# Optimization experiments

Hardware: AMD Instinct MI355X
Metric: run time of the kernel (lower is better)

The kernel has to match this reference:

```python
import jax, jax.numpy as jnp
import numpy as np

N_NODES = 50000
N_EDGES = 800000
N_GRAPHS = 512
NODE_IN = 128
EDGE_IN = 64
HIDDEN = 128
SHARED = 64


def setup_inputs() -> dict:
    key = jax.random.key(0)
    ks = jax.random.split(key, 24)
    def lin(k, fan_in, fan_out):
        lim = 1.0 / np.sqrt(fan_in)
        kw, kb = jax.random.split(k)
        w = jax.random.uniform(kw, (fan_in, fan_out), jnp.float32, -lim, lim)
        b = jax.random.uniform(kb, (fan_out,), jnp.float32, -lim, lim)
        return w, b
    x = jax.random.normal(ks[0], (N_NODES, NODE_IN), jnp.float32)
    edge_index = jax.random.randint(ks[1], (2, N_EDGES), 0, N_NODES, jnp.int64)
    edge_attr = jax.random.normal(ks[2], (N_EDGES, EDGE_IN), jnp.float32)
    batch = jnp.sort(jax.random.randint(ks[3], (N_NODES,), 0, N_GRAPHS, jnp.int64))
    e1_w, e1_b = lin(ks[4], EDGE_IN, NODE_IN)
    n1_w1, n1_b1 = lin(ks[5], NODE_IN, HIDDEN)
    n1_w2, n1_b2 = lin(ks[6], HIDDEN, HIDDEN)
    e2_w, e2_b = lin(ks[7], EDGE_IN, HIDDEN)
    n2_w1, n2_b1 = lin(ks[8], HIDDEN, HIDDEN)
    n2_w2, n2_b2 = lin(ks[9], HIDDEN, HIDDEN)
    fc_w, fc_b = lin(ks[10], HIDDEN, SHARED)
    hS_w, hS_b = lin(ks[11], SHARED, 1)
    hP_w, hP_b = lin(ks[12], SHARED, 1)
    hN_w, hN_b = lin(ks[13], SHARED, 1)
    return dict(x=x, edge_index=edge_index, edge_attr=edge_attr, batch=batch,
                e1_w=e1_w, e1_b=e1_b, n1_w1=n1_w1, n1_b1=n1_b1, n1_w2=n1_w2, n1_b2=n1_b2,
                e2_w=e2_w, e2_b=e2_b, n2_w1=n2_w1, n2_b1=n2_b1, n2_w2=n2_w2, n2_b2=n2_b2,
                fc_w=fc_w, fc_b=fc_b, hS_w=hS_w, hS_b=hS_b, hP_w=hP_w, hP_b=hP_b,
                hN_w=hN_w, hN_b=hN_b)


def gine_conv(x, edge_index, edge_attr, ew, eb, w1, b1, w2, b2):
    # message: relu(x_j + Lin(edge_attr)); aggregate: scatter-sum to target;
    # update: MLP((1 + eps) * x_i + aggr) with eps = 0 (PyG default)
    e = edge_attr @ ew + eb                      # [E, C]
    m = jax.nn.relu(x[edge_index[0]] + e)        # gather + fused add/relu
    aggr = jax.ops.segment_sum(m, edge_index[1], num_segments=N_NODES)
    h = x + aggr
    return jax.nn.relu(h @ w1 + b1) @ w2 + b2


def global_mean_pool(x, batch):
    sums = jax.ops.segment_sum(x, batch, num_segments=N_GRAPHS)
    cnt = jax.ops.segment_sum(jnp.ones((x.shape[0],), x.dtype), batch, num_segments=N_GRAPHS)
    return sums / jnp.maximum(cnt, 1.0)[:, None]


def reference(x, edge_index, edge_attr, batch,
              e1_w, e1_b, n1_w1, n1_b1, n1_w2, n1_b2,
              e2_w, e2_b, n2_w1, n2_b1, n2_w2, n2_b2,
              fc_w, fc_b, hS_w, hS_b, hP_w, hP_b, hN_w, hN_b):
    h = jax.nn.relu(gine_conv(x, edge_index, edge_attr, e1_w, e1_b, n1_w1, n1_b1, n1_w2, n1_b2))
    h = jax.nn.relu(gine_conv(h, edge_index, edge_attr, e2_w, e2_b, n2_w1, n2_b1, n2_w2, n2_b2))
    g = global_mean_pool(h, batch)               # [G, HIDDEN]
    s = jax.nn.relu(g @ fc_w + fc_b)             # [G, SHARED]
    logS = (s @ hS_w + hS_b)[:, 0]
    logP = (s @ hP_w + hP_b)[:, 0]
    nr = (s @ hN_w + hN_b)[:, 0]
    return logS, logP, nr
```

## Files before the change

### kernel.cpp

```cpp
#include <hip/hip_runtime.h>
#include <hip/hip_bf16.h>


typedef __bf16 bf16_t;

#define N_NODES   50000
#define N_EDGES   800000
#define N_GRAPHS  512
#define HID       128
#define EIN       64
#define PNODES    16
#define SCAN_BLK  1024
#define NCHUNK    49

#define RL(v, l)  __int_as_float(__builtin_amdgcn_readlane(__float_as_int(v), (l)))
#define RLI(v, l) __builtin_amdgcn_readlane((v), (l))

__device__ __forceinline__ float ldf(const void* p, size_t i, int f32m) {
    return f32m ? ((const float*)p)[i] : (float)((const bf16_t*)p)[i];
}
__device__ __forceinline__ int ldi(const void* p, size_t i, int i64m) {
    return i64m ? (int)((const long long*)p)[i] : ((const int*)p)[i];
}

__global__ void k_detect(const unsigned short* __restrict__ xw,
                         const unsigned int*   __restrict__ eiw,
                         int* __restrict__ flags)
{
    if (threadIdx.x == 0 && blockIdx.x == 0) {
        int sane = 0;
        for (int i = 0; i < 256; ++i) {
            int e = (xw[i] >> 7) & 0xFF;
            if (e >= 100 && e <= 150) ++sane;
        }
        flags[0] = (sane < 220) ? 1 : 0;
        int nzhigh = 0;
        for (int i = 0; i < 256; ++i)
            if (eiw[2*i + 1] != 0) ++nzhigh;
        flags[1] = (nzhigh == 0) ? 1 : 0;
    }
}

__global__ void k_cvt4(const void* __restrict__ x, float* __restrict__ dst,
                       const int* __restrict__ flags) {
    const int f32m = flags[0];
    size_t i = (size_t)blockIdx.x * 256 + threadIdx.x;
    if (f32m) {
        ((float4*)dst)[i] = ((const float4*)x)[i];
    } else {
        const bf16_t* s = (const bf16_t*)x;
        float4 v;
        v.x = (float)s[4*i+0]; v.y = (float)s[4*i+1];
        v.z = (float)s[4*i+2]; v.w = (float)s[4*i+3];
        ((float4*)dst)[i] = v;
    }
}

__global__ void k_hist(const void* __restrict__ ei, int* __restrict__ CNT,
                       const int* __restrict__ flags)
{
    const int i64m = flags[1];
    int e = blockIdx.x * 256 + threadIdx.x;
    int d = ldi(ei, (size_t)N_EDGES + e, i64m);
    atomicAdd(&CNT[d], 1);
}

__global__ __launch_bounds__(SCAN_BLK) void k_scanA(const int* __restrict__ CNT,
                                                    int* __restrict__ OFF,
                                                    int* __restrict__ PS)
{
    __shared__ int tmp[SCAN_BLK];
    const int t = threadIdx.x;
    const int i = blockIdx.x * SCAN_BLK + t;
    const int v = (i < N_NODES) ? CNT[i] : 0;
    tmp[t] = v;
    __syncthreads();
    for (int off = 1; off < SCAN_BLK; off <<= 1) {
        int u = (t >= off) ? tmp[t - off] : 0;
        __syncthreads();
        tmp[t] += u;
        __syncthreads();
    }
    if (i < N_NODES) OFF[i] = tmp[t] - v;
    if (t == SCAN_BLK - 1) PS[blockIdx.x] = tmp[t];
}

__global__ void k_scanB(int* __restrict__ PS)
{
    const int lane = threadIdx.x;
    const int v0 = (lane < NCHUNK) ? PS[lane] : 0;
    int v = v0;
#pragma unroll
    for (int off = 1; off < 64; off <<= 1) {
        int u = __shfl_up(v, off, 64);
        if (lane >= off) v += u;
    }
    if (lane < NCHUNK) PS[lane] = v - v0;
}

__global__ void k_scanC(int* __restrict__ OFF, const int* __restrict__ PS,
                        int* __restrict__ CUR)
{
    int i = blockIdx.x * 256 + threadIdx.x;
    if (i < N_NODES) {
        int o = OFF[i] + PS[i >> 10];
        OFF[i] = o;
        CUR[i] = o;
    }
}

__global__ void k_scatter(const void* __restrict__ ei, int* __restrict__ CUR,
                          int* __restrict__ CSR, const int* __restrict__ flags)
{
    const int i64m = flags[1];
    int e = blockIdx.x * 256 + threadIdx.x;
    int s = ldi(ei, e, i64m);
    int d = ldi(ei, (size_t)N_EDGES + e, i64m);
    int p = atomicAdd(&CUR[d], 1);
    CSR[p]              = e;
    CSR[N_EDGES + p]    = s;
    CSR[2*N_EDGES + p]  = d;
}

__global__ __launch_bounds__(512) void k_edge_s(
        const void* __restrict__ Xg, int xg_ws,
        const int*  __restrict__ CSR,
        const void* __restrict__ ea,
        const void* __restrict__ ew,
        const void* __restrict__ eb,
        float*      __restrict__ ag,
        const int*  __restrict__ flags)
{
    __shared__ float4 Wq[16 * 128];
    __shared__ float  ebs[HID];
    const int f32m = flags[0];
    const int xgf  = xg_ws ? 1 : f32m;

    for (int i = threadIdx.x; i < 16 * 128; i += 512) {
        int k4 = i >> 7, c = i & 127;
        float4 w;
        w.x = ldf(ew, (size_t)(4*k4+0)*HID + c, f32m);
        w.y = ldf(ew, (size_t)(4*k4+1)*HID + c, f32m);
        w.z = ldf(ew, (size_t)(4*k4+2)*HID + c, f32m);
        w.w = ldf(ew, (size_t)(4*k4+3)*HID + c, f32m);
        Wq[i] = w;
    }
    for (int i = threadIdx.x; i < HID; i += 512) ebs[i] = ldf(eb, i, f32m);
    __syncthreads();

    const int lane = threadIdx.x & 63;
    const int wid  = (blockIdx.x * 512 + threadIdx.x) >> 6;
    const int nw   = gridDim.x * 8;
    const int ngrp = N_EDGES / 8;
    const float eb0 = ebs[lane], eb1 = ebs[64 + lane];

    auto LOADIDX = [&](int p0) -> int {
        int v = 0;
        if (lane < 24) v = CSR[(size_t)(lane >> 3) * N_EDGES + p0 + (lane & 7)];
        return v;
    };
    auto LOADAV = [&](int vv, float* av) {
#pragma unroll
        for (int i = 0; i < 8; ++i) {
            int eid = RLI(vv, i);
            av[i] = ldf(ea, (size_t)eid * EIN + lane, f32m);
        }
    };

    int g = wid;
    if (g < ngrp) {
        float avA[8];
        int vvA = LOADIDX(g * 8);
        LOADAV(vvA, avA);
        int gB = g + nw;
        int vvB = (gB < ngrp) ? LOADIDX(gB * 8) : 0;

        while (true) {
            const bool hasB = (gB < ngrp);
            float avB[8];
            if (hasB) LOADAV(vvB, avB);
            const int gC = gB + nw;
            int vvC = (hasB && gC < ngrp) ? LOADIDX(gC * 8) : 0;

            int src[8], dst[8];
#pragma unroll
            for (int i = 0; i < 8; ++i) {
                src[i] = RLI(vvA, 8 + i);
                dst[i] = RLI(vvA, 16 + i);
            }
            float x0[8], x1[8];
#pragma unroll
            for (int i = 0; i < 8; ++i) {
                x0[i] = ldf(Xg, (size_t)src[i] * HID + lane,      xgf);
                x1[i] = ldf(Xg, (size_t)src[i] * HID + 64 + lane, xgf);
            }

            float acc0[8], acc1[8];
#pragma unroll
            for (int i = 0; i < 8; ++i) { acc0[i] = 0.f; acc1[i] = 0.f; }

#pragma unroll 4
            for (int k4 = 0; k4 < 16; ++k4) {
                float4 w0 = Wq[k4 * 128 + lane];
                float4 w1 = Wq[k4 * 128 + 64 + lane];
#pragma unroll
                for (int i = 0; i < 8; ++i) {
                    float a0 = RL(avA[i], 4*k4+0);
                    float a1 = RL(avA[i], 4*k4+1);
                    float a2 = RL(avA[i], 4*k4+2);
                    float a3 = RL(avA[i], 4*k4+3);
                    acc0[i] = fmaf(a3, w0.w, fmaf(a2, w0.z, fmaf(a1, w0.y, fmaf(a0, w0.x, acc0[i]))));
                    acc1[i] = fmaf(a3, w1.w, fmaf(a2, w1.z, fmaf(a1, w1.y, fmaf(a0, w1.x, acc1[i]))));
                }
            }

            float s0 = 0.f, s1 = 0.f;
#pragma unroll
            for (int i = 0; i < 8; ++i) {
                float v0 = fmaxf(x0[i] + acc0[i] + eb0, 0.f);
                float v1 = fmaxf(x1[i] + acc1[i] + eb1, 0.f);
                s0 += v0; s1 += v1;
                if (i == 7 || dst[i + 1] != dst[i]) {
                    unsafeAtomicAdd(ag + (size_t)dst[i] * HID + lane,      s0);
                    unsafeAtomicAdd(ag + (size_t)dst[i] * HID + 64 + lane, s1);
                    s0 = 0.f; s1 = 0.f;
                }
            }

            if (!hasB) break;
            g = gB; gB = gC;
            vvA = vvB; vvB = vvC;
#pragma unroll
            for (int i = 0; i < 8; ++i) avA[i] = avB[i];
        }
    }
}

__global__ __launch_bounds__(1024) void k_mlp2(
        const float* __restrict__ A,
        const void*  __restrict__ W1, const void* __restrict__ b1,
        const void*  __restrict__ W2, const void* __restrict__ b2,
        float*       __restrict__ Out,
        float*       __restrict__ Out2,
        const int*   __restrict__ flags)
{
    __shared__ float4 W1q[32 * 128];
    __shared__ float4 W2q[32 * 128];
    const int f32m = flags[0];
    for (int i = threadIdx.x; i < 32 * 128; i += 1024) {
        int k4 = i >> 7, c = i & 127;
        float4 w;
        w.x = ldf(W1, (size_t)(4*k4+0)*HID + c, f32m);
        w.y = ldf(W1, (size_t)(4*k4+1)*HID + c, f32m);
        w.z = ldf(W1, (size_t)(4*k4+2)*HID + c, f32m);
        w.w = ldf(W1, (size_t)(4*k4+3)*HID + c, f32m);
        W1q[i] = w;
        w.x = ldf(W2, (size_t)(4*k4+0)*HID + c, f32m);
        w.y = ldf(W2, (size_t)(4*k4+1)*HID + c, f32m);
        w.z = ldf(W2, (size_t)(4*k4+2)*HID + c, f32m);
        w.w = ldf(W2, (size_t)(4*k4+3)*HID + c, f32m);
        W2q[i] = w;
    }
    __syncthreads();

    const int lane = threadIdx.x & 63;
    const int wid  = (blockIdx.x * 1024 + threadIdx.x) >> 6;
    const int nw   = gridDim.x * 16;
    const float c10 = ldf(b1, lane,      f32m);
    const float c11 = ldf(b1, 64 + lane, f32m);
    const float c20 = ldf(b2, lane,      f32m);
    const float c21 = ldf(b2, 64 + lane, f32m);
    const int ngrp = N_NODES / 8;

    for (int g = wid; g < ngrp; g += nw) {
        const int n0 = g * 8;
        float alo[8], ahi[8], t0[8], t1[8];
#pragma unroll
        for (int i = 0; i < 8; ++i) {
            alo[i] = A[(size_t)(n0+i) * HID + lane];
            ahi[i] = A[(size_t)(n0+i) * HID + 64 + lane];
            t0[i] = c10; t1[i] = c11;
        }
#pragma unroll 4
        for (int k4 = 0; k4 < 16; ++k4) {
            float4 w0 = W1q[k4 * 128 + lane];
            float4 w1 = W1q[k4 * 128 + 64 + lane];
#pragma unroll
            for (int i = 0; i < 8; ++i) {
                float a0 = RL(alo[i], 4*k4+0);
                float a1 = RL(alo[i], 4*k4+1);
                float a2 = RL(alo[i], 4*k4+2);
                float a3 = RL(alo[i], 4*k4+3);
                t0[i] = fmaf(a3, w0.w, fmaf(a2, w0.z, fmaf(a1, w0.y, fmaf(a0, w0.x, t0[i]))));
                t1[i] = fmaf(a3, w1.w, fmaf(a2, w1.z, fmaf(a1, w1.y, fmaf(a0, w1.x, t1[i]))));
            }
        }
#pragma unroll 4
        for (int k4 = 16; k4 < 32; ++k4) {
            float4 w0 = W1q[k4 * 128 + lane];
            float4 w1 = W1q[k4 * 128 + 64 + lane];
#pragma unroll
            for (int i = 0; i < 8; ++i) {
                float a0 = RL(ahi[i], 4*k4+0 - 64);
                float a1 = RL(ahi[i], 4*k4+1 - 64);
                float a2 = RL(ahi[i], 4*k4+2 - 64);
                float a3 = RL(ahi[i], 4*k4+3 - 64);
                t0[i] = fmaf(a3, w0.w, fmaf(a2, w0.z, fmaf(a1, w0.y, fmaf(a0, w0.x, t0[i]))));
                t1[i] = fmaf(a3, w1.w, fmaf(a2, w1.z, fmaf(a1, w1.y, fmaf(a0, w1.x, t1[i]))));
            }
        }
#pragma unroll
        for (int i = 0; i < 8; ++i) {
            t0[i] = fmaxf(t0[i], 0.f);
            t1[i] = fmaxf(t1[i], 0.f);
        }
        float o0[8], o1[8];
#pragma unroll
        for (int i = 0; i < 8; ++i) { o0[i] = c20; o1[i] = c21; }
#pragma unroll 4
        for (int k4 = 0; k4 < 16; ++k4) {
            float4 w0 = W2q[k4 * 128 + lane];
            float4 w1 = W2q[k4 * 128 + 64 + lane];
#pragma unroll
            for (int i = 0; i < 8; ++i) {
                float a0 = RL(t0[i], 4*k4+0);
                float a1 = RL(t0[i], 4*k4+1);
                float a2 = RL(t0[i], 4*k4+2);
                float a3 = RL(t0[i], 4*k4+3);
                o0[i] = fmaf(a3, w0.w, fmaf(a2, w0.z, fmaf(a1, w0.y, fmaf(a0, w0.x, o0[i]))));
                o1[i] = fmaf(a3, w1.w, fmaf(a2, w1.z, fmaf(a1, w1.y, fmaf(a0, w1.x, o1[i]))));
            }
        }
#pragma unroll 4
        for (int k4 = 16; k4 < 32; ++k4) {
            float4 w0 = W2q[k4 * 128 + lane];
            float4 w1 = W2q[k4 * 128 + 64 + lane];
#pragma unroll
            for (int i = 0; i < 8; ++i) {
                float a0 = RL(t1[i], 4*k4+0 - 64);
                float a1 = RL(t1[i], 4*k4+1 - 64);
                float a2 = RL(t1[i], 4*k4+2 - 64);
                float a3 = RL(t1[i], 4*k4+3 - 64);
                o0[i] = fmaf(a3, w0.w, fmaf(a2, w0.z, fmaf(a1, w0.y, fmaf(a0, w0.x, o0[i]))));
                o1[i] = fmaf(a3, w1.w, fmaf(a2, w1.z, fmaf(a1, w1.y, fmaf(a0, w1.x, o1[i]))));
            }
        }
#pragma unroll
        for (int i = 0; i < 8; ++i) {
            float v0 = fmaxf(o0[i], 0.f);
            float v1 = fmaxf(o1[i], 0.f);
            Out[(size_t)(n0+i) * HID + lane]      = v0;
            Out[(size_t)(n0+i) * HID + 64 + lane] = v1;
            if (Out2) {
                Out2[(size_t)(n0+i) * HID + lane]      = v0;
                Out2[(size_t)(n0+i) * HID + 64 + lane] = v1;
            }
        }
    }
}

__global__ void k_pool_s(const float* __restrict__ X, const void* __restrict__ batch,
                         float* __restrict__ GS, float* __restrict__ GC,
                         const int* __restrict__ flags)
{
    const int i64m = flags[1];
    const int c  = threadIdx.x;
    const int tl = threadIdx.x & 63;
    const int n0 = blockIdx.x * PNODES;

    int bv = (tl < PNODES) ? ldi(batch, n0 + tl, i64m) : 0;

    int bprev = RLI(bv, 0);
    float acc = 0.f;
    int   cnt = 0;
#pragma unroll
    for (int j = 0; j < PNODES; ++j) {
        int b = RLI(bv, j);
        if (b != bprev) {
            unsafeAtomicAdd(&GS[(size_t)bprev * HID + c], acc);
            if (c == 0) unsafeAtomicAdd(&GC[bprev], (float)cnt);
            acc = 0.f; cnt = 0; bprev = b;
        }
        acc += X[(size_t)(n0 + j) * HID + c];
        ++cnt;
    }
    unsafeAtomicAdd(&GS[(size_t)bprev * HID + c], acc);
    if (c == 0) unsafeAtomicAdd(&GC[bprev], (float)cnt);
}

__global__ void k_head(const float* __restrict__ GS, const float* __restrict__ GC,
                       const void* __restrict__ fcw, const void* __restrict__ fcb,
                       const void* __restrict__ hSw, const void* __restrict__ hSb,
                       const void* __restrict__ hPw, const void* __restrict__ hPb,
                       const void* __restrict__ hNw, const void* __restrict__ hNb,
                       float* __restrict__ out, const int* __restrict__ flags)
{
    const int f32m = flags[0];
    const int g = blockIdx.x;
    const int lane = threadIdx.x;
    const float inv = 1.f / fmaxf(GC[g], 1.f);
    const float g0 = GS[(size_t)g * HID + lane]      * inv;
    const float g1 = GS[(size_t)g * HID + 64 + lane] * inv;

    float acc = 0.f;
    for (int k = 0; k < 64; ++k) {
        float gk = __shfl(g0, k, 64);
        acc += gk * ldf(fcw, k * 64 + lane, f32m);
    }
    for (int k = 0; k < 64; ++k) {
        float gk = __shfl(g1, k, 64);
        acc += gk * ldf(fcw, (64 + k) * 64 + lane, f32m);
    }
    float s = fmaxf(acc + ldf(fcb, lane, f32m), 0.f);

    float pS = s * ldf(hSw, lane, f32m);
    float pP = s * ldf(hPw, lane, f32m);
    float pN = s * ldf(hNw, lane, f32m);
#pragma unroll
    for (int off = 32; off; off >>= 1) {
        pS += __shfl_down(pS, off, 64);
        pP += __shfl_down(pP, off, 64);
        pN += __shfl_down(pN, off, 64);
    }
    if (lane == 0) {
        out[g]                = pS + ldf(hSb, 0, f32m);
        out[N_GRAPHS + g]     = pP + ldf(hPb, 0, f32m);
        out[2 * N_GRAPHS + g] = pN + ldf(hNb, 0, f32m);
    }
}

extern "C" void kernel_launch(void* const* d_in, const int* in_sizes, int n_in,
                              void* d_out, int out_size, void* d_ws, size_t ws_size,
                              hipStream_t stream)
{
    const void* x     = d_in[0];
    const void* ei    = d_in[1];
    const void* ea    = d_in[2];
    const void* batch = d_in[3];
    const void* e1w = d_in[4],  *e1b = d_in[5];
    const void* n1w1= d_in[6],  *n1b1= d_in[7];
    const void* n1w2= d_in[8],  *n1b2= d_in[9];
    const void* e2w = d_in[10], *e2b = d_in[11];
    const void* n2w1= d_in[12], *n2b1= d_in[13];
    const void* n2w2= d_in[14], *n2b2= d_in[15];
    const void* fcw = d_in[16], *fcb = d_in[17];
    const void* hSw = d_in[18], *hSb = d_in[19];
    const void* hPw = d_in[20], *hPb = d_in[21];
    const void* hNw = d_in[22], *hNb = d_in[23];

    float* B1  = (float*)d_ws;
    float* B2  = B1 + (size_t)N_NODES * HID;
    float* GS  = B2 + (size_t)N_NODES * HID;
    float* GC  = GS + (size_t)N_GRAPHS * HID;
    int*   FL  = (int*)(GC + N_GRAPHS);
    int*   PS  = FL + 4;
    int*   OFF = PS + 64;
    int*   CNT = OFF + N_NODES;
    int*   CUR = CNT + N_NODES;
    int*   CSR = CUR + N_NODES;

    k_detect<<<1, 64, 0, stream>>>((const unsigned short*)x, (const unsigned int*)ei, FL);
    hipMemsetAsync(GS, 0, (N_GRAPHS * HID + N_GRAPHS) * sizeof(float), stream);
    hipMemsetAsync(CNT, 0, N_NODES * sizeof(int), stream);

    k_hist   <<<N_EDGES / 256, 256, 0, stream>>>(ei, CNT, FL);
    k_scanA  <<<NCHUNK, SCAN_BLK, 0, stream>>>(CNT, OFF, PS);
    k_scanB  <<<1, 64, 0, stream>>>(PS);
    k_scanC  <<<(N_NODES + 255) / 256, 256, 0, stream>>>(OFF, PS, CUR);
    k_scatter<<<N_EDGES / 256, 256, 0, stream>>>(ei, CUR, CSR, FL);

    const int NV4_BLKS = (N_NODES * HID / 4) / 256;

    k_cvt4  <<<NV4_BLKS, 256, 0, stream>>>(x, B1, FL);
    k_edge_s<<<2048, 512, 0, stream>>>(x, 0, CSR, ea, e1w, e1b, B1, FL);
    k_mlp2  <<<256, 1024, 0, stream>>>(B1, n1w1, n1b1, n1w2, n1b2, B1, B2, FL);

    k_edge_s<<<2048, 512, 0, stream>>>(B1, 1, CSR, ea, e2w, e2b, B2, FL);
    k_mlp2  <<<256, 1024, 0, stream>>>(B2, n2w1, n2b1, n2w2, n2b2, B2, nullptr, FL);

    k_pool_s<<<N_NODES / PNODES, 128, 0, stream>>>(B2, batch, GS, GC, FL);
    k_head  <<<N_GRAPHS, 64, 0, stream>>>(GS, GC, fcw, fcb, hSw, hSb, hPw, hPb, hNw, hNb,
                                          (float*)d_out, FL);
}
```

Baseline: 1.261 ms.

## Hold GEMM weights in registers and split node MLP into per-layer kernels

```diff
diff --git a/kernel.cpp b/kernel.cpp
--- a/kernel.cpp
+++ b/kernel.cpp
@@ -122,7 +122,7 @@
     CSR[2*N_EDGES + p]  = d;
 }
 
-__global__ __launch_bounds__(512) void k_edge_s(
+__global__ __launch_bounds__(256, 2) void k_edge_r(
         const void* __restrict__ Xg, int xg_ws,
         const int*  __restrict__ CSR,
         const void* __restrict__ ea,
@@ -131,28 +131,31 @@
         float*      __restrict__ ag,
         const int*  __restrict__ flags)
 {
-    __shared__ float4 Wq[16 * 128];
-    __shared__ float  ebs[HID];
     const int f32m = flags[0];
     const int xgf  = xg_ws ? 1 : f32m;
-
-    for (int i = threadIdx.x; i < 16 * 128; i += 512) {
-        int k4 = i >> 7, c = i & 127;
-        float4 w;
-        w.x = ldf(ew, (size_t)(4*k4+0)*HID + c, f32m);
-        w.y = ldf(ew, (size_t)(4*k4+1)*HID + c, f32m);
-        w.z = ldf(ew, (size_t)(4*k4+2)*HID + c, f32m);
-        w.w = ldf(ew, (size_t)(4*k4+3)*HID + c, f32m);
-        Wq[i] = w;
-    }
-    for (int i = threadIdx.x; i < HID; i += 512) ebs[i] = ldf(eb, i, f32m);
-    __syncthreads();
-
     const int lane = threadIdx.x & 63;
-    const int wid  = (blockIdx.x * 512 + threadIdx.x) >> 6;
-    const int nw   = gridDim.x * 8;
+    const int wid  = (blockIdx.x * 256 + threadIdx.x) >> 6;
+    const int nw   = gridDim.x * 4;
     const int ngrp = N_EDGES / 8;
-    const float eb0 = ebs[lane], eb1 = ebs[64 + lane];
+
+    float wr0[EIN], wr1[EIN];
+    if (f32m) {
+        const float* Wf = (const float*)ew;
+#pragma unroll
+        for (int k = 0; k < EIN; ++k) {
+            wr0[k] = Wf[(size_t)k * HID + lane];
+            wr1[k] = Wf[(size_t)k * HID + 64 + lane];
+        }
+    } else {
+        const bf16_t* Wb = (const bf16_t*)ew;
+#pragma unroll
+        for (int k = 0; k < EIN; ++k) {
+            wr0[k] = (float)Wb[(size_t)k * HID + lane];
+            wr1[k] = (float)Wb[(size_t)k * HID + 64 + lane];
+        }
+    }
+    const float eb0 = ldf(eb, lane,      f32m);
+    const float eb1 = ldf(eb, 64 + lane, f32m);
 
     auto LOADIDX = [&](int p0) -> int {
         int v = 0;
@@ -199,18 +202,18 @@
 #pragma unroll
             for (int i = 0; i < 8; ++i) { acc0[i] = 0.f; acc1[i] = 0.f; }
 
-#pragma unroll 4
+#pragma unroll
             for (int k4 = 0; k4 < 16; ++k4) {
-                float4 w0 = Wq[k4 * 128 + lane];
-                float4 w1 = Wq[k4 * 128 + 64 + lane];
 #pragma unroll
                 for (int i = 0; i < 8; ++i) {
                     float a0 = RL(avA[i], 4*k4+0);
                     float a1 = RL(avA[i], 4*k4+1);
                     float a2 = RL(avA[i], 4*k4+2);
                     float a3 = RL(avA[i], 4*k4+3);
-                    acc0[i] = fmaf(a3, w0.w, fmaf(a2, w0.z, fmaf(a1, w0.y, fmaf(a0, w0.x, acc0[i]))));
-                    acc1[i] = fmaf(a3, w1.w, fmaf(a2, w1.z, fmaf(a1, w1.y, fmaf(a0, w1.x, acc1[i]))));
+                    acc0[i] = fmaf(a3, wr0[4*k4+3], fmaf(a2, wr0[4*k4+2],
+                              fmaf(a1, wr0[4*k4+1], fmaf(a0, wr0[4*k4+0], acc0[i]))));
+                    acc1[i] = fmaf(a3, wr1[4*k4+3], fmaf(a2, wr1[4*k4+2],
+                              fmaf(a1, wr1[4*k4+1], fmaf(a0, wr1[4*k4+0], acc1[i]))));
                 }
             }
 
@@ -236,119 +239,97 @@
     }
 }
 
-__global__ __launch_bounds__(1024) void k_mlp2(
+__global__ __launch_bounds__(256, 2) void k_mlp_r(
         const float* __restrict__ A,
-        const void*  __restrict__ W1, const void* __restrict__ b1,
-        const void*  __restrict__ W2, const void* __restrict__ b2,
+        const void*  __restrict__ W,
+        const void*  __restrict__ bias,
         float*       __restrict__ Out,
         float*       __restrict__ Out2,
         const int*   __restrict__ flags)
 {
-    __shared__ float4 W1q[32 * 128];
-    __shared__ float4 W2q[32 * 128];
     const int f32m = flags[0];
-    for (int i = threadIdx.x; i < 32 * 128; i += 1024) {
-        int k4 = i >> 7, c = i & 127;
-        float4 w;
-        w.x = ldf(W1, (size_t)(4*k4+0)*HID + c, f32m);
-        w.y = ldf(W1, (size_t)(4*k4+1)*HID + c, f32m);
-        w.z = ldf(W1, (size_t)(4*k4+2)*HID + c, f32m);
-        w.w = ldf(W1, (size_t)(4*k4+3)*HID + c, f32m);
-        W1q[i] = w;
-        w.x = ldf(W2, (size_t)(4*k4+0)*HID + c, f32m);
-        w.y = ldf(W2, (size_t)(4*k4+1)*HID + c, f32m);
-        w.z = ldf(W2, (size_t)(4*k4+2)*HID + c, f32m);
-        w.w = ldf(W2, (size_t)(4*k4+3)*HID + c, f32m);
-        W2q[i] = w;
-    }
-    __syncthreads();
-
     const int lane = threadIdx.x & 63;
-    const int wid  = (blockIdx.x * 1024 + threadIdx.x) >> 6;
-    const int nw   = gridDim.x * 16;
-    const float c10 = ldf(b1, lane,      f32m);
-    const float c11 = ldf(b1, 64 + lane, f32m);
-    const float c20 = ldf(b2, lane,      f32m);
-    const float c21 = ldf(b2, 64 + lane, f32m);
+    const int wid  = (blockIdx.x * 256 + threadIdx.x) >> 6;
+    const int nw   = gridDim.x * 4;
+    const float b0 = ldf(bias, lane,      f32m);
+    const float b1 = ldf(bias, 64 + lane, f32m);
     const int ngrp = N_NODES / 8;
+
+    const float*  Wf = (const float*)W;
+    const bf16_t* Wb = (const bf16_t*)W;
+
+    float wr0[64], wr1[64];
 
     for (int g = wid; g < ngrp; g += nw) {
         const int n0 = g * 8;
-        float alo[8], ahi[8], t0[8], t1[8];
+        float alo[8], ahi[8], acc0[8], acc1[8];
 #pragma unroll
         for (int i = 0; i < 8; ++i) {
             alo[i] = A[(size_t)(n0+i) * HID + lane];
             ahi[i] = A[(size_t)(n0+i) * HID + 64 + lane];
-            t0[i] = c10; t1[i] = c11;
-        }
-#pragma unroll 4
+            acc0[i] = b0; acc1[i] = b1;
+        }
+
+        if (f32m) {
+#pragma unroll
+            for (int k = 0; k < 64; ++k) {
+                wr0[k] = Wf[(size_t)k * HID + lane];
+                wr1[k] = Wf[(size_t)k * HID + 64 + lane];
+            }
+        } else {
+#pragma unroll
+            for (int k = 0; k < 64; ++k) {
+                wr0[k] = (float)Wb[(size_t)k * HID + lane];
+                wr1[k] = (float)Wb[(size_t)k * HID + 64 + lane];
+            }
+        }
+#pragma unroll
         for (int k4 = 0; k4 < 16; ++k4) {
-            float4 w0 = W1q[k4 * 128 + lane];
-            float4 w1 = W1q[k4 * 128 + 64 + lane];
 #pragma unroll
             for (int i = 0; i < 8; ++i) {
                 float a0 = RL(alo[i], 4*k4+0);
                 float a1 = RL(alo[i], 4*k4+1);
                 float a2 = RL(alo[i], 4*k4+2);
                 float a3 = RL(alo[i], 4*k4+3);
-                t0[i] = fmaf(a3, w0.w, fmaf(a2, w0.z, fmaf(a1, w0.y, fmaf(a0, w0.x, t0[i]))));
-                t1[i] = fmaf(a3, w1.w, fmaf(a2, w1.z, fmaf(a1, w1.y, fmaf(a0, w1.x, t1[i]))));
-            }
-        }
-#pragma unroll 4
-        for (int k4 = 16; k4 < 32; ++k4) {
-            float4 w0 = W1q[k4 * 128 + lane];
-            float4 w1 = W1q[k4 * 128 + 64 + lane];
+                acc0[i] = fmaf(a3, wr0[4*k4+3], fmaf(a2, wr0[4*k4+2],
+                          fmaf(a1, wr0[4*k4+1], fmaf(a0, wr0[4*k4+0], acc0[i]))));
+                acc1[i] = fmaf(a3, wr1[4*k4+3], fmaf(a2, wr1[4*k4+2],
+                          fmaf(a1, wr1[4*k4+1], fmaf(a0, wr1[4*k4+0], acc1[i]))));
+            }
+        }
+
+        if (f32m) {
+#pragma unroll
+            for (int k = 0; k < 64; ++k) {
+                wr0[k] = Wf[(size_t)(64 + k) * HID + lane];
+                wr1[k] = Wf[(size_t)(64 + k) * HID + 64 + lane];
+            }
+        } else {
+#pragma unroll
+            for (int k = 0; k < 64; ++k) {
+                wr0[k] = (float)Wb[(size_t)(64 + k) * HID + lane];
+                wr1[k] = (float)Wb[(size_t)(64 + k) * HID + 64 + lane];
+            }
+        }
+#pragma unroll
+        for (int k4 = 0; k4 < 16; ++k4) {
 #pragma unroll
             for (int i = 0; i < 8; ++i) {
-                float a0 = RL(ahi[i], 4*k4+0 - 64);
-                float a1 = RL(ahi[i], 4*k4+1 - 64);
-                float a2 = RL(ahi[i], 4*k4+2 - 64);
-                float a3 = RL(ahi[i], 4*k4+3 - 64);
-                t0[i] = fmaf(a3, w0.w, fmaf(a2, w0.z, fmaf(a1, w0.y, fmaf(a0, w0.x, t0[i]))));
-                t1[i] = fmaf(a3, w1.w, fmaf(a2, w1.z, fmaf(a1, w1.y, fmaf(a0, w1.x, t1[i]))));
-            }
-        }
+                float a0 = RL(ahi[i], 4*k4+0);
+                float a1 = RL(ahi[i], 4*k4+1);
+                float a2 = RL(ahi[i], 4*k4+2);
+                float a3 = RL(ahi[i], 4*k4+3);
+                acc0[i] = fmaf(a3, wr0[4*k4+3], fmaf(a2, wr0[4*k4+2],
+                          fmaf(a1, wr0[4*k4+1], fmaf(a0, wr0[4*k4+0], acc0[i]))));
+                acc1[i] = fmaf(a3, wr1[4*k4+3], fmaf(a2, wr1[4*k4+2],
+                          fmaf(a1, wr1[4*k4+1], fmaf(a0, wr1[4*k4+0], acc1[i]))));
+            }
+        }
+
 #pragma unroll
         for (int i = 0; i < 8; ++i) {
-            t0[i] = fmaxf(t0[i], 0.f);
-            t1[i] = fmaxf(t1[i], 0.f);
-        }
-        float o0[8], o1[8];
-#pragma unroll
-        for (int i = 0; i < 8; ++i) { o0[i] = c20; o1[i] = c21; }
-#pragma unroll 4
-        for (int k4 = 0; k4 < 16; ++k4) {
-            float4 w0 = W2q[k4 * 128 + lane];
-            float4 w1 = W2q[k4 * 128 + 64 + lane];
-#pragma unroll
-            for (int i = 0; i < 8; ++i) {
-                float a0 = RL(t0[i], 4*k4+0);
-                float a1 = RL(t0[i], 4*k4+1);
-                float a2 = RL(t0[i], 4*k4+2);
-                float a3 = RL(t0[i], 4*k4+3);
-                o0[i] = fmaf(a3, w0.w, fmaf(a2, w0.z, fmaf(a1, w0.y, fmaf(a0, w0.x, o0[i]))));
-                o1[i] = fmaf(a3, w1.w, fmaf(a2, w1.z, fmaf(a1, w1.y, fmaf(a0, w1.x, o1[i]))));
-            }
-        }
-#pragma unroll 4
-        for (int k4 = 16; k4 < 32; ++k4) {
-            float4 w0 = W2q[k4 * 128 + lane];
-            float4 w1 = W2q[k4 * 128 + 64 + lane];
-#pragma unroll
-            for (int i = 0; i < 8; ++i) {
-                float a0 = RL(t1[i], 4*k4+0 - 64);
-                float a1 = RL(t1[i], 4*k4+1 - 64);
-                float a2 = RL(t1[i], 4*k4+2 - 64);
-                float a3 = RL(t1[i], 4*k4+3 - 64);
-                o0[i] = fmaf(a3, w0.w, fmaf(a2, w0.z, fmaf(a1, w0.y, fmaf(a0, w0.x, o0[i]))));
-                o1[i] = fmaf(a3, w1.w, fmaf(a2, w1.z, fmaf(a1, w1.y, fmaf(a0, w1.x, o1[i]))));
-            }
-        }
-#pragma unroll
-        for (int i = 0; i < 8; ++i) {
-            float v0 = fmaxf(o0[i], 0.f);
-            float v1 = fmaxf(o1[i], 0.f);
+            float v0 = fmaxf(acc0[i], 0.f);
+            float v1 = fmaxf(acc1[i], 0.f);
             Out[(size_t)(n0+i) * HID + lane]      = v0;
             Out[(size_t)(n0+i) * HID + 64 + lane] = v1;
             if (Out2) {
@@ -472,11 +453,13 @@
     const int NV4_BLKS = (N_NODES * HID / 4) / 256;
 
     k_cvt4  <<<NV4_BLKS, 256, 0, stream>>>(x, B1, FL);
-    k_edge_s<<<2048, 512, 0, stream>>>(x, 0, CSR, ea, e1w, e1b, B1, FL);
-    k_mlp2  <<<256, 1024, 0, stream>>>(B1, n1w1, n1b1, n1w2, n1b2, B1, B2, FL);
-
-    k_edge_s<<<2048, 512, 0, stream>>>(B1, 1, CSR, ea, e2w, e2b, B2, FL);
-    k_mlp2  <<<256, 1024, 0, stream>>>(B2, n2w1, n2b1, n2w2, n2b2, B2, nullptr, FL);
+    k_edge_r<<<512, 256, 0, stream>>>(x, 0, CSR, ea, e1w, e1b, B1, FL);
+    k_mlp_r <<<512, 256, 0, stream>>>(B1, n1w1, n1b1, B1, nullptr, FL);
+    k_mlp_r <<<512, 256, 0, stream>>>(B1, n1w2, n1b2, B1, B2, FL);
+
+    k_edge_r<<<512, 256, 0, stream>>>(B1, 1, CSR, ea, e2w, e2b, B2, FL);
+    k_mlp_r <<<512, 256, 0, stream>>>(B2, n2w1, n2b1, B2, nullptr, FL);
+    k_mlp_r <<<512, 256, 0, stream>>>(B2, n2w2, n2b2, B2, nullptr, FL);
 
     k_pool_s<<<N_NODES / PNODES, 128, 0, stream>>>(B2, batch, GS, GC, FL);
     k_head  <<<N_GRAPHS, 64, 0, stream>>>(GS, GC, fcw, fcb, hSw, hSb, hPw, hPb, hNw, hNb,
```

After: 4.500 ms. 257% more time.
